# Optimization experiments

Measured on AMD Instinct MI355X. Metric: run time of the kernel, lower is better.

The kernel has to match this reference:

```python
import jax, jax.numpy as jnp
import numpy as np

D_MODEL = 2048
DOWN = 512
UP = 1024
NUM_HEADS = 16
ROPE_DIM = 64
BS = 16
SEQ = 512
BASE = 10000.0
HEAD_DIM = D_MODEL // NUM_HEADS          # 128 (used only in the softmax scale)
V_HEAD_DIM = UP // NUM_HEADS             # 64


def _linear(x, W, b):
    # torch nn.Linear: y = x @ W.T + b, W shape (out, in)
    return x @ W.T + b


def _rope(x, num_heads, rope_dim):
    # Faithful to source RotaryEmbedding, including the swapped sin/cos caches:
    #   cos_pos = sin(pos*theta), sin_pos = cos(pos*theta)
    bs, L, _ = x.shape
    q = x.reshape(bs, L, num_heads, rope_dim).transpose(0, 2, 1, 3)  # (bs,h,L,d)
    theta = 1.0 / (BASE ** (jnp.arange(0, rope_dim, 2, dtype=jnp.float32) / rope_dim))
    ang = jnp.arange(L, dtype=jnp.float32)[:, None] * theta[None, :]   # (L, d/2)
    cos_pos = jnp.repeat(jnp.sin(ang), 2, axis=-1)  # (L, d) -- source quirk
    sin_pos = jnp.repeat(jnp.cos(ang), 2, axis=-1)
    q2 = jnp.stack([-q[..., 1::2], q[..., ::2]], axis=-1).reshape(bs, num_heads, L, rope_dim)
    return q * cos_pos + q2 * sin_pos


def setup_inputs() -> dict:
    key = jax.random.key(0)
    ks = jax.random.split(key, 18)
    s = 0.02
    d = {
        "h": jax.random.normal(ks[0], (BS, SEQ, D_MODEL), jnp.float32),
        "W_down_kv": jax.random.normal(ks[1], (DOWN, D_MODEL), jnp.float32) * s,
        "b_down_kv": jnp.zeros((DOWN,), jnp.float32),
        "W_up_k": jax.random.normal(ks[2], (UP, DOWN), jnp.float32) * s,
        "b_up_k": jnp.zeros((UP,), jnp.float32),
        "W_up_v": jax.random.normal(ks[3], (UP, DOWN), jnp.float32) * s,
        "b_up_v": jnp.zeros((UP,), jnp.float32),
        "W_down_q": jax.random.normal(ks[4], (DOWN, D_MODEL), jnp.float32) * s,
        "b_down_q": jnp.zeros((DOWN,), jnp.float32),
        "W_up_q": jax.random.normal(ks[5], (UP, DOWN), jnp.float32) * s,
        "b_up_q": jnp.zeros((UP,), jnp.float32),
        "W_qr": jax.random.normal(ks[6], (ROPE_DIM * NUM_HEADS, DOWN), jnp.float32) * s,
        "b_qr": jnp.zeros((ROPE_DIM * NUM_HEADS,), jnp.float32),
        "W_kr": jax.random.normal(ks[7], (ROPE_DIM, D_MODEL), jnp.float32) * s,
        "b_kr": jnp.zeros((ROPE_DIM,), jnp.float32),
        "W_fc": jax.random.normal(ks[8], (D_MODEL, NUM_HEADS * V_HEAD_DIM), jnp.float32) * s,
        "b_fc": jnp.zeros((D_MODEL,), jnp.float32),
    }
    return d


def reference(h, W_down_kv, b_down_kv, W_up_k, b_up_k, W_up_v, b_up_v,
              W_down_q, b_down_q, W_up_q, b_up_q, W_qr, b_qr,
              W_kr, b_kr, W_fc, b_fc):
    bs, L, _ = h.shape
    # low-rank KV path
    c_kv = _linear(h, W_down_kv, b_down_kv)             # (bs,L,down)
    k_c = _linear(c_kv, W_up_k, b_up_k)                 # (bs,L,up)
    v_c = _linear(c_kv, W_up_v, b_up_v)                 # (bs,L,up)
    # low-rank Q path
    c_q = _linear(h, W_down_q, b_down_q)                # (bs,L,down)
    q_c = _linear(c_q, W_up_q, b_up_q)                  # (bs,L,up)
    # rope (decoupled) path
    q_r = _rope(_linear(c_q, W_qr, b_qr), NUM_HEADS, ROPE_DIM)  # (bs,H,L,rope)
    k_r = _rope(_linear(h, W_kr, b_kr), 1, ROPE_DIM)            # (bs,1,L,rope)

    q_c = q_c.reshape(bs, L, NUM_HEADS, -1).transpose(0, 2, 1, 3)  # (bs,H,L,64)
    q = jnp.concatenate([q_c, q_r], axis=-1)                        # (bs,H,L,128)
    k_c = k_c.reshape(bs, L, NUM_HEADS, -1).transpose(0, 2, 1, 3)
    k_r = jnp.broadcast_to(k_r, (bs, NUM_HEADS, L, ROPE_DIM))       # shared across heads
    k = jnp.concatenate([k_c, k_r], axis=-1)

    scale = 1.0 / jnp.sqrt(jnp.float32(HEAD_DIM + ROPE_DIM))  # sqrt(192), per source
    scores = jnp.einsum('bhqd,bhkd->bhqk', q, k) * scale
    attn = jax.nn.softmax(scores, axis=-1)  # dropout is identity in eval mode

    v = v_c.reshape(bs, L, NUM_HEADS, V_HEAD_DIM).transpose(0, 2, 1, 3)
    out = jnp.einsum('bhqk,bhkd->bhqd', attn, v)
    out = out.transpose(0, 2, 1, 3).reshape(bs, L, -1)   # (bs,L,H*v_head_dim)
    return _linear(out, W_fc, b_fc)                      # (bs,L,d_model)
```

## Files before the change

kernel.cpp:

```cpp
#include <hip/hip_runtime.h>
#include <hip/hip_bf16.h>

typedef __bf16 bf16x8 __attribute__((ext_vector_type(8)));
typedef float f32x4 __attribute__((ext_vector_type(4)));
using u16 = unsigned short;
using u32 = unsigned int;

__device__ __forceinline__ float bf2f(u16 v) {
    unsigned int u = (unsigned int)v << 16;
    float f; __builtin_memcpy(&f, &u, 4); return f;
}
__device__ __forceinline__ u16 f2bf(float f) {
    unsigned int u; __builtin_memcpy(&u, &f, 4);
    u += 0x7FFFu + ((u >> 16) & 1u);
    return (u16)(u >> 16);
}

struct Cvt9 {
    const float* src[9];
    u16* dst[9];
    int end[9];
};
__global__ __launch_bounds__(256) void cvt_all(Cvt9 d, int total)
{
    int c = blockIdx.x * 256 + threadIdx.x;
    if (c >= total) return;
    int seg = 0;
    while (c >= d.end[seg]) ++seg;
    int local = c - (seg ? d.end[seg - 1] : 0);
    const float* s = d.src[seg] + (size_t)local * 8;
    float4 f0 = *(const float4*)s;
    float4 f1 = *(const float4*)(s + 4);
    u16 tmp[8] = { f2bf(f0.x), f2bf(f0.y), f2bf(f0.z), f2bf(f0.w),
                   f2bf(f1.x), f2bf(f1.y), f2bf(f1.z), f2bf(f1.w) };
    *(uint4*)(d.dst[seg] + (size_t)local * 8) = *(const uint4*)tmp;
}

struct Cpy7 {
    const float* src[7];
    float* dst[7];
    int end[7];
};
__global__ __launch_bounds__(256) void copy_f32(Cpy7 d, int total)
{
    int c = blockIdx.x * 256 + threadIdx.x;
    if (c >= total) return;
    int seg = 0;
    while (c >= d.end[seg]) ++seg;
    int local = c - (seg ? d.end[seg - 1] : 0);
    d.dst[seg][local] = d.src[seg][local];
}

template<bool CF>
__global__ __launch_bounds__(256) void gemm_v6(
    const u16* __restrict__ A0, const u16* __restrict__ B0, void* __restrict__ C0, const float* __restrict__ e0,
    const u16* __restrict__ A1, const u16* __restrict__ B1, void* __restrict__ C1, const float* __restrict__ e1,
    int ysplit, int lda, int ldb, int ldc, int N, int K)
{
    __shared__ __align__(16) u16 As[3][128 * 32];
    __shared__ __align__(16) u16 Bs[3][128 * 32];

    const int t = threadIdx.x;
    const int lane = t & 63;
    const int w = t >> 6;
    const int wm = w >> 1, wn = w & 1;
    const int l16 = lane & 15, quad = lane >> 4;
    const int m0 = blockIdx.x * 128;

    const u16* A; const u16* B; void* Cv; const float* bias; int yl;
    if ((int)blockIdx.y < ysplit) { A = A0; B = B0; Cv = C0; bias = e0; yl = blockIdx.y; }
    else                          { A = A1; B = B1; Cv = C1; bias = e1; yl = blockIdx.y - ysplit; }
    const int n0 = yl * 128;

    const int sub  = lane >> 2;
    const int slot = lane & 3;
    const int agc  = slot ^ ((sub >> 1) & 3);
    const int sfr  = (l16 >> 1) & 3;

    f32x4 acc[4][4];
#pragma unroll
    for (int i = 0; i < 4; ++i)
#pragma unroll
        for (int j = 0; j < 4; ++j) acc[i][j] = (f32x4){0.f, 0.f, 0.f, 0.f};

    auto STAGE = [&](int buf, int k0) {
#pragma unroll
        for (int c = 0; c < 2; ++c) {
            const int rr = w * 32 + c * 16;
            const u16* ga = A + (size_t)(m0 + rr + sub) * lda + k0 + agc * 8;
            __builtin_amdgcn_global_load_lds(
                (const __attribute__((address_space(1))) u32*)ga,
                (__attribute__((address_space(3))) u32*)&As[buf][rr * 32], 16, 0, 0);
            const u16* gb = B + (size_t)(n0 + rr + sub) * ldb + k0 + agc * 8;
            __builtin_amdgcn_global_load_lds(
                (const __attribute__((address_space(1))) u32*)gb,
                (__attribute__((address_space(3))) u32*)&Bs[buf][rr * 32], 16, 0, 0);
        }
    };

    const int nt = K >> 5;
    STAGE(0, 0);
    STAGE(1, 32);
    int cur = 0;
    for (int tt = 0; tt < nt; ++tt) {
        int pre = cur + 2; if (pre >= 3) pre -= 3;
        if (tt + 2 < nt) {
            STAGE(pre, (tt + 2) << 5);
            asm volatile("s_waitcnt vmcnt(8)");
        } else if (tt + 1 < nt) {
            asm volatile("s_waitcnt vmcnt(4)");
        } else {
            asm volatile("s_waitcnt vmcnt(0)");
        }
        __builtin_amdgcn_s_barrier();

        const u16* Ab = As[cur];
        bf16x8 af[4], bfr[4];
#pragma unroll
        for (int i = 0; i < 4; ++i)
            af[i] = *(const bf16x8*)&Ab[(wm * 64 + i * 16 + l16) * 32 + (quad ^ sfr) * 8];
#pragma unroll
        for (int j = 0; j < 4; ++j)
            bfr[j] = *(const bf16x8*)&Bs[cur][(wn * 64 + j * 16 + l16) * 32 + (quad ^ sfr) * 8];
#pragma unroll
        for (int i = 0; i < 4; ++i)
#pragma unroll
            for (int j = 0; j < 4; ++j)
                acc[i][j] = __builtin_amdgcn_mfma_f32_16x16x32_bf16(bfr[j], af[i], acc[i][j], 0, 0, 0);

        __builtin_amdgcn_s_barrier();
        cur += 1; if (cur >= 3) cur -= 3;
    }

#pragma unroll
    for (int i = 0; i < 4; ++i) {
        const int row = m0 + wm * 64 + i * 16 + l16;
#pragma unroll
        for (int j = 0; j < 4; ++j) {
            const int colb = n0 + wn * 64 + j * 16 + quad * 4;
            if (colb >= N) continue;
            float4 bv = *(const float4*)&bias[colb];
            float v0 = acc[i][j][0] + bv.x;
            float v1 = acc[i][j][1] + bv.y;
            float v2 = acc[i][j][2] + bv.z;
            float v3 = acc[i][j][3] + bv.w;
            if (CF) {
                float4 out = { v0, v1, v2, v3 };
                *(float4*)((float*)Cv + (size_t)row * ldc + colb) = out;
            } else {
                u16 p[4] = { f2bf(v0), f2bf(v1), f2bf(v2), f2bf(v3) };
                *(uint2*)((u16*)Cv + (size_t)row * ldc + colb) = *(const uint2*)p;
            }
        }
    }
}

__global__ void rope_inplace(u16* __restrict__ buf, int ld, int col0, int ppr, int total)
{
    int idx = blockIdx.x * 256 + threadIdx.x;
    if (idx >= total) return;
    int row = idx / ppr;
    int pi  = idx - row * ppr;
    int grp = pi >> 5;
    int i   = pi & 31;
    int pos = row & 511;
    float theta = __expf(-(float)i * 0.2878231366242558f);
    float ang = (float)pos * theta;
    float s = sinf(ang), c = cosf(ang);
    size_t base = (size_t)row * ld + col0 + grp * 64 + 2 * i;
    float x0 = bf2f(buf[base]);
    float x1 = bf2f(buf[base + 1]);
    buf[base]     = f2bf(x0 * s - x1 * c);
    buf[base + 1] = f2bf(x1 * s + x0 * c);
}

__global__ __launch_bounds__(256) void attn_kernel(
    const u16* __restrict__ q_src,
    const u16* __restrict__ kv_src,
    const u16* __restrict__ kr_src,
    u16* __restrict__ o_dst, int ldo)
{
    __shared__ __align__(16) u16 Ks[64 * 136];
    __shared__ __align__(16) u16 Vt[64 * 72];
    __shared__ __align__(16) u16 Ps[64 * 72];

    const int t = threadIdx.x;
    const int lane = t & 63;
    const int w = t >> 6;
    const int l16 = lane & 15, quad = lane >> 4;
    const int a7 = l16 & 7;

    const int id   = blockIdx.x;
    const int xcd  = id & 7;
    const int qt   = (id >> 3) & 7;
    const int panel = xcd + ((id >> 6) << 3);
    const int h = panel & 15;
    const int b = panel >> 4;
    const int qrow0 = b * 512 + qt * 64;
    const int krow_base = b * 512;

    bf16x8 aq[4];
    {
        const u16* qrow = q_src + (size_t)(qrow0 + w * 16 + l16) * 2048;
#pragma unroll
        for (int ks = 0; ks < 4; ++ks) {
            int col = ks * 32 + quad * 8;
            const u16* src = (col < 64) ? qrow + h * 64 + col
                                        : qrow + 1024 + h * 64 + (col - 64);
            aq[ks] = *(const bf16x8*)src;
        }
    }

    const int colK = (t & 15) * 8;
    const int r0k  = t >> 4;
    const u16* kbase; int kstr;
    if (colK < 64) { kbase = kv_src + h * 64 + colK;        kstr = 2048; }
    else           { kbase = kr_src + 1024 + (colK - 64);   kstr = 1088; }
    u16* kw = &Ks[r0k * 136 + colK];

    const int v00 = (t & 7) * 8;
    const int r0v = t >> 3;
    const u16* vbase = kv_src + 1024 + h * 64 + v00;
    const int rotA = (r0v + v00) & 63;
    const int rotB = (r0v + 32 + v00) & 63;
    u16* vwA = &Vt[v00 * 72 + rotA];
    u16* vwB = &Vt[v00 * 72 + rotB];

    auto LOADT = [&](int krow0, uint4& K0, uint4& K1, uint4& K2, uint4& K3,
                     uint4& V0, uint4& V1) {
        K0 = *(const uint4*)(kbase + (size_t)(krow0 + r0k     ) * kstr);
        K1 = *(const uint4*)(kbase + (size_t)(krow0 + r0k + 16) * kstr);
        K2 = *(const uint4*)(kbase + (size_t)(krow0 + r0k + 32) * kstr);
        K3 = *(const uint4*)(kbase + (size_t)(krow0 + r0k + 48) * kstr);
        V0 = *(const uint4*)(vbase + (size_t)(krow0 + r0v     ) * 2048);
        V1 = *(const uint4*)(vbase + (size_t)(krow0 + r0v + 32) * 2048);
    };
    auto WRITET = [&](const uint4& K0, const uint4& K1, const uint4& K2, const uint4& K3,
                      const uint4& V0, const uint4& V1) {
        *(uint4*)(kw)            = K0;
        *(uint4*)(kw + 16 * 136) = K1;
        *(uint4*)(kw + 32 * 136) = K2;
        *(uint4*)(kw + 48 * 136) = K3;
        u16 ta[8], tb[8];
        __builtin_memcpy(ta, &V0, 16);
        __builtin_memcpy(tb, &V1, 16);
#pragma unroll
        for (int j2 = 0; j2 < 8; ++j2) { vwA[j2 * 72] = ta[j2]; vwB[j2 * 72] = tb[j2]; }
    };

    float m2 = -1e30f, l_run = 0.f;
    f32x4 o[4];
#pragma unroll
    for (int n = 0; n < 4; ++n) o[n] = (f32x4){0.f, 0.f, 0.f, 0.f};

    const float C = 0.10411756f;

    uint4 kA0, kA1, kA2, kA3, vA0, vA1;
    uint4 kB0, kB1, kB2, kB3, vB0, vB1;
    LOADT(krow_base, kA0, kA1, kA2, kA3, vA0, vA1);

    for (int kt = 0; kt < 8; ++kt) {
        __builtin_amdgcn_s_barrier();
        if ((kt & 1) == 0) {
            WRITET(kA0, kA1, kA2, kA3, vA0, vA1);
            if (kt < 7) LOADT(krow_base + (kt + 1) * 64, kB0, kB1, kB2, kB3, vB0, vB1);
        } else {
            WRITET(kB0, kB1, kB2, kB3, vB0, vB1);
            if (kt < 7) LOADT(krow_base + (kt + 1) * 64, kA0, kA1, kA2, kA3, vA0, vA1);
        }
        asm volatile("s_waitcnt lgkmcnt(0)");
        __builtin_amdgcn_sched_barrier(0);
        __builtin_amdgcn_s_barrier();

        f32x4 s[4];
#pragma unroll
        for (int n = 0; n < 4; ++n) s[n] = (f32x4){0.f, 0.f, 0.f, 0.f};
#pragma unroll
        for (int ks = 0; ks < 4; ++ks) {
#pragma unroll
            for (int n = 0; n < 4; ++n) {
                bf16x8 bk = *(const bf16x8*)&Ks[(n * 16 + l16) * 136 + ks * 32 + quad * 8];
                s[n] = __builtin_amdgcn_mfma_f32_16x16x32_bf16(bk, aq[ks], s[n], 0, 0, 0);
            }
        }

        float mx = fmaxf(fmaxf(s[0][0], s[0][1]), fmaxf(s[0][2], s[0][3]));
#pragma unroll
        for (int n = 1; n < 4; ++n)
            mx = fmaxf(mx, fmaxf(fmaxf(s[n][0], s[n][1]), fmaxf(s[n][2], s[n][3])));
        mx = fmaxf(mx, __shfl_xor(mx, 16));
        mx = fmaxf(mx, __shfl_xor(mx, 32));

        float mnew = fmaxf(m2, mx * C);
        float alpha = __builtin_amdgcn_exp2f(m2 - mnew);
        m2 = mnew;
        float rs = 0.f;
#pragma unroll
        for (int n = 0; n < 4; ++n)
#pragma unroll
            for (int r = 0; r < 4; ++r) {
                float pv = __builtin_amdgcn_exp2f(__builtin_fmaf(s[n][r], C, -mnew));
                s[n][r] = pv;
                rs += pv;
            }
        rs += __shfl_xor(rs, 16);
        rs += __shfl_xor(rs, 32);
        l_run = l_run * alpha + rs;

        float aO[4];
#pragma unroll
        for (int r = 0; r < 4; ++r) aO[r] = __shfl(alpha, quad * 4 + r);
#pragma unroll
        for (int n = 0; n < 4; ++n)
#pragma unroll
            for (int r = 0; r < 4; ++r) o[n][r] *= aO[r];

        {
            u16* prow = &Ps[(w * 16 + l16) * 72];
#pragma unroll
            for (int n = 0; n < 4; ++n) {
                int p = (2 * n + (quad >> 1) + a7) & 7;
                u32 p0 = (u32)f2bf(s[n][0]) | ((u32)f2bf(s[n][1]) << 16);
                u32 p1 = (u32)f2bf(s[n][2]) | ((u32)f2bf(s[n][3]) << 16);
                uint2 pp = { p0, p1 };
                *(uint2*)&prow[p * 8 + (quad & 1) * 4] = pp;
            }
        }

#pragma unroll
        for (int kk = 0; kk < 2; ++kk) {
            bf16x8 ap = *(const bf16x8*)&Ps[(w * 16 + l16) * 72
                          + (((4 * kk + quad + a7) & 7) << 3)];
#pragma unroll
            for (int n = 0; n < 4; ++n) {
                bf16x8 bv = *(const bf16x8*)&Vt[(n * 16 + l16) * 72
                              + ((kk * 32 + quad * 8 + n * 16 + (l16 & 8)) & 63)];
                o[n] = __builtin_amdgcn_mfma_f32_16x16x32_bf16(ap, bv, o[n], 0, 0, 0);
            }
        }
    }

    float inv = 1.0f / l_run;
#pragma unroll
    for (int r = 0; r < 4; ++r) {
        float invO = __shfl(inv, quad * 4 + r);
        int row = qrow0 + w * 16 + quad * 4 + r;
#pragma unroll
        for (int n = 0; n < 4; ++n) {
            int col = h * 64 + n * 16 + l16;
            o_dst[(size_t)row * ldo + col] = f2bf(o[n][r] * invO);
        }
    }
}

extern "C" void kernel_launch(void* const* d_in, const int* in_sizes, int n_in,
                              void* d_out, int out_size, void* d_ws, size_t ws_size,
                              hipStream_t stream)
{
    const float* h    = (const float*)d_in[0];
    const float* Wdkv = (const float*)d_in[1];
    const float* bdkv = (const float*)d_in[2];
    const float* Wuk  = (const float*)d_in[3];
    const float* buk  = (const float*)d_in[4];
    const float* Wuv  = (const float*)d_in[5];
    const float* buv  = (const float*)d_in[6];
    const float* Wdq  = (const float*)d_in[7];
    const float* bdq  = (const float*)d_in[8];
    const float* Wuq  = (const float*)d_in[9];
    const float* buq  = (const float*)d_in[10];
    const float* Wqr  = (const float*)d_in[11];
    const float* bqr  = (const float*)d_in[12];
    const float* Wkr  = (const float*)d_in[13];
    const float* bkr  = (const float*)d_in[14];
    const float* Wfc  = (const float*)d_in[15];
    const float* bfc  = (const float*)d_in[16];

    char* ws = (char*)d_ws;
    u16* out1   = (u16*)ws;
    u16* hbf    = (u16*)(ws + 17825792);
    u16* out2a  = hbf;
    u16* out2b  = (u16*)(ws + 51380224);
    u16* w1     = (u16*)(ws + 84934656);
    u16* w2a    = (u16*)(ws + 89653248);
    u16* w2b    = (u16*)(ws + 91750400);
    u16* wfc    = (u16*)(ws + 93847552);
    float* bias_s1 = (float*)(ws + 98041856);
    float* bias_2  = (float*)(ws + 98046208);

    Cvt9 cd;
    const float* srcs[9] = { h, Wdkv, Wdq, Wkr, Wuk, Wuv, Wuq, Wqr, Wfc };
    u16* dsts[9] = { hbf, w1, w1 + 512 * 2048, w1 + 1024 * 2048,
                     w2a, w2a + 1024 * 512, w2b, w2b + 1024 * 512, wfc };
    int cnts[9] = { 2097152, 131072, 131072, 16384, 65536, 65536, 65536, 65536, 262144 };
    int acc2 = 0;
    for (int i = 0; i < 9; ++i) { cd.src[i] = srcs[i]; cd.dst[i] = dsts[i]; acc2 += cnts[i]; cd.end[i] = acc2; }
    cvt_all<<<(acc2 + 255) / 256, 256, 0, stream>>>(cd, acc2);
    hipMemsetAsync(w1 + 1088 * 2048, 0, 64 * 2048 * sizeof(u16), stream);

    Cpy7 bc;
    const float* bs[7] = { bdkv, bdq, bkr, buk, buv, buq, bqr };
    float* bd[7] = { bias_s1, bias_s1 + 512, bias_s1 + 1024,
                     bias_2, bias_2 + 1024, bias_2 + 2048, bias_2 + 3072 };
    int bn[7] = { 512, 512, 64, 1024, 1024, 1024, 1024 };
    int bacc = 0;
    for (int i = 0; i < 7; ++i) { bc.src[i] = bs[i]; bc.dst[i] = bd[i]; bacc += bn[i]; bc.end[i] = bacc; }
    copy_f32<<<(bacc + 255) / 256, 256, 0, stream>>>(bc, bacc);

    gemm_v6<false><<<dim3(64, 9), 256, 0, stream>>>(
        hbf, w1, out1, bias_s1,
        hbf, w1, out1, bias_s1, 9, 2048, 2048, 1088, 1088, 2048);
    rope_inplace<<<1024, 256, 0, stream>>>(out1, 1088, 1024, 32, 8192 * 32);

    gemm_v6<false><<<dim3(64, 32), 256, 0, stream>>>(
        out1,       w2a, out2a, bias_2,
        out1 + 512, w2b, out2b, bias_2 + 2048, 16, 1088, 512, 2048, 2048, 512);
    rope_inplace<<<16384, 256, 0, stream>>>(out2b, 2048, 1024, 512, 8192 * 512);

    attn_kernel<<<2048, 256, 0, stream>>>(out2b, out2a, out1, out1, 1088);

    gemm_v6<true><<<dim3(64, 16), 256, 0, stream>>>(
        out1, wfc, d_out, bfc,
        out1, wfc, d_out, bfc, 16, 1088, 1024, 2048, 2048, 1024);
}
```

Measured before the change: 414.3 us.

## Fuse RoPE into GEMM epilogues, widen attention blocks, skip rescale when max stable

The two standalone rope_inplace passes are removed, and RoPE is applied in the GEMM epilogue to columns at or above 1024, computed in fp32 before the bf16 rounding. The attention kernel now runs 512 threads over 128 query rows, so each K/V tile is shared by twice as many queries and each thread issues fewer loads. The online softmax skips the max update and output rescale when the new tile max stays within a threshold of the running max, trading exactness of the running max for fewer exp and multiply operations. These changes remove extra memory passes and kernel launches, but the lazy-rescale threshold risks overflow or precision loss if scores jump sharply.

```diff
diff --git a/kernel.cpp b/kernel.cpp
--- a/kernel.cpp
+++ b/kernel.cpp
@@ -52,10 +52,10 @@
 }
 
 template<bool CF>
-__global__ __launch_bounds__(256) void gemm_v6(
+__global__ __launch_bounds__(256) void gemm_v7(
     const u16* __restrict__ A0, const u16* __restrict__ B0, void* __restrict__ C0, const float* __restrict__ e0,
     const u16* __restrict__ A1, const u16* __restrict__ B1, void* __restrict__ C1, const float* __restrict__ e1,
-    int ysplit, int lda, int ldb, int ldc, int N, int K)
+    int ysplit, int lda, int ldb, int ldc, int N, int K, int rp0, int rp1)
 {
     __shared__ __align__(16) u16 As[3][128 * 32];
     __shared__ __align__(16) u16 Bs[3][128 * 32];
@@ -67,9 +67,9 @@
     const int l16 = lane & 15, quad = lane >> 4;
     const int m0 = blockIdx.x * 128;
 
-    const u16* A; const u16* B; void* Cv; const float* bias; int yl;
-    if ((int)blockIdx.y < ysplit) { A = A0; B = B0; Cv = C0; bias = e0; yl = blockIdx.y; }
-    else                          { A = A1; B = B1; Cv = C1; bias = e1; yl = blockIdx.y - ysplit; }
+    const u16* A; const u16* B; void* Cv; const float* bias; int yl; int rp;
+    if ((int)blockIdx.y < ysplit) { A = A0; B = B0; Cv = C0; bias = e0; yl = blockIdx.y; rp = rp0; }
+    else                          { A = A1; B = B1; Cv = C1; bias = e1; yl = blockIdx.y - ysplit; rp = rp1; }
     const int n0 = yl * 128;
 
     const int sub  = lane >> 2;
@@ -144,6 +144,21 @@
             float v1 = acc[i][j][1] + bv.y;
             float v2 = acc[i][j][2] + bv.z;
             float v3 = acc[i][j][3] + bv.w;
+            if (rp && colb >= 1024) {
+                const float LN = 0.2878231366242558f;
+                int i0 = ((colb - 1024) & 63) >> 1;
+                float th0 = __expf(-(float)i0 * LN);
+                float th1 = __expf(-(float)(i0 + 1) * LN);
+                float ps = (float)(row & 511);
+                float a0 = ps * th0, a1 = ps * th1;
+                float s0 = sinf(a0), c0 = cosf(a0);
+                float s1 = sinf(a1), c1 = cosf(a1);
+                float t0 = v0 * s0 - v1 * c0;
+                float t1 = v1 * s0 + v0 * c0;
+                float t2 = v2 * s1 - v3 * c1;
+                float t3 = v3 * s1 + v2 * c1;
+                v0 = t0; v1 = t1; v2 = t2; v3 = t3;
+            }
             if (CF) {
                 float4 out = { v0, v1, v2, v3 };
                 *(float4*)((float*)Cv + (size_t)row * ldc + colb) = out;
@@ -155,26 +170,7 @@
     }
 }
 
-__global__ void rope_inplace(u16* __restrict__ buf, int ld, int col0, int ppr, int total)
-{
-    int idx = blockIdx.x * 256 + threadIdx.x;
-    if (idx >= total) return;
-    int row = idx / ppr;
-    int pi  = idx - row * ppr;
-    int grp = pi >> 5;
-    int i   = pi & 31;
-    int pos = row & 511;
-    float theta = __expf(-(float)i * 0.2878231366242558f);
-    float ang = (float)pos * theta;
-    float s = sinf(ang), c = cosf(ang);
-    size_t base = (size_t)row * ld + col0 + grp * 64 + 2 * i;
-    float x0 = bf2f(buf[base]);
-    float x1 = bf2f(buf[base + 1]);
-    buf[base]     = f2bf(x0 * s - x1 * c);
-    buf[base + 1] = f2bf(x1 * s + x0 * c);
-}
-
-__global__ __launch_bounds__(256) void attn_kernel(
+__global__ __launch_bounds__(512) void attn_kernel(
     const u16* __restrict__ q_src,
     const u16* __restrict__ kv_src,
     const u16* __restrict__ kr_src,
@@ -182,7 +178,7 @@
 {
     __shared__ __align__(16) u16 Ks[64 * 136];
     __shared__ __align__(16) u16 Vt[64 * 72];
-    __shared__ __align__(16) u16 Ps[64 * 72];
+    __shared__ __align__(16) u16 Ps[128 * 72];
 
     const int t = threadIdx.x;
     const int lane = t & 63;
@@ -192,11 +188,11 @@
 
     const int id   = blockIdx.x;
     const int xcd  = id & 7;
-    const int qt   = (id >> 3) & 7;
-    const int panel = xcd + ((id >> 6) << 3);
+    const int qt   = (id >> 3) & 3;
+    const int panel = xcd + ((id >> 5) << 3);
     const int h = panel & 15;
     const int b = panel >> 4;
-    const int qrow0 = b * 512 + qt * 64;
+    const int qrow0 = b * 512 + qt * 128;
     const int krow_base = b * 512;
 
     bf16x8 aq[4];
@@ -222,30 +218,20 @@
     const int r0v = t >> 3;
     const u16* vbase = kv_src + 1024 + h * 64 + v00;
     const int rotA = (r0v + v00) & 63;
-    const int rotB = (r0v + 32 + v00) & 63;
     u16* vwA = &Vt[v00 * 72 + rotA];
-    u16* vwB = &Vt[v00 * 72 + rotB];
-
-    auto LOADT = [&](int krow0, uint4& K0, uint4& K1, uint4& K2, uint4& K3,
-                     uint4& V0, uint4& V1) {
+
+    auto LOADT = [&](int krow0, uint4& K0, uint4& K1, uint4& V0) {
         K0 = *(const uint4*)(kbase + (size_t)(krow0 + r0k     ) * kstr);
-        K1 = *(const uint4*)(kbase + (size_t)(krow0 + r0k + 16) * kstr);
-        K2 = *(const uint4*)(kbase + (size_t)(krow0 + r0k + 32) * kstr);
-        K3 = *(const uint4*)(kbase + (size_t)(krow0 + r0k + 48) * kstr);
+        K1 = *(const uint4*)(kbase + (size_t)(krow0 + r0k + 32) * kstr);
         V0 = *(const uint4*)(vbase + (size_t)(krow0 + r0v     ) * 2048);
-        V1 = *(const uint4*)(vbase + (size_t)(krow0 + r0v + 32) * 2048);
     };
-    auto WRITET = [&](const uint4& K0, const uint4& K1, const uint4& K2, const uint4& K3,
-                      const uint4& V0, const uint4& V1) {
+    auto WRITET = [&](const uint4& K0, const uint4& K1, const uint4& V0) {
         *(uint4*)(kw)            = K0;
-        *(uint4*)(kw + 16 * 136) = K1;
-        *(uint4*)(kw + 32 * 136) = K2;
-        *(uint4*)(kw + 48 * 136) = K3;
-        u16 ta[8], tb[8];
+        *(uint4*)(kw + 32 * 136) = K1;
+        u16 ta[8];
         __builtin_memcpy(ta, &V0, 16);
-        __builtin_memcpy(tb, &V1, 16);
-#pragma unroll
-        for (int j2 = 0; j2 < 8; ++j2) { vwA[j2 * 72] = ta[j2]; vwB[j2 * 72] = tb[j2]; }
+#pragma unroll
+        for (int j2 = 0; j2 < 8; ++j2) vwA[j2 * 72] = ta[j2];
     };
 
     float m2 = -1e30f, l_run = 0.f;
@@ -254,19 +240,20 @@
     for (int n = 0; n < 4; ++n) o[n] = (f32x4){0.f, 0.f, 0.f, 0.f};
 
     const float C = 0.10411756f;
-
-    uint4 kA0, kA1, kA2, kA3, vA0, vA1;
-    uint4 kB0, kB1, kB2, kB3, vB0, vB1;
-    LOADT(krow_base, kA0, kA1, kA2, kA3, vA0, vA1);
+    const float THR2 = 11.5419f;
+
+    uint4 kA0, kA1, vA0;
+    uint4 kB0, kB1, vB0;
+    LOADT(krow_base, kA0, kA1, vA0);
 
     for (int kt = 0; kt < 8; ++kt) {
         __builtin_amdgcn_s_barrier();
         if ((kt & 1) == 0) {
-            WRITET(kA0, kA1, kA2, kA3, vA0, vA1);
-            if (kt < 7) LOADT(krow_base + (kt + 1) * 64, kB0, kB1, kB2, kB3, vB0, vB1);
+            WRITET(kA0, kA1, vA0);
+            if (kt < 7) LOADT(krow_base + (kt + 1) * 64, kB0, kB1, vB0);
         } else {
-            WRITET(kB0, kB1, kB2, kB3, vB0, vB1);
-            if (kt < 7) LOADT(krow_base + (kt + 1) * 64, kA0, kA1, kA2, kA3, vA0, vA1);
+            WRITET(kB0, kB1, vB0);
+            if (kt < 7) LOADT(krow_base + (kt + 1) * 64, kA0, kA1, vA0);
         }
         asm volatile("s_waitcnt lgkmcnt(0)");
         __builtin_amdgcn_sched_barrier(0);
@@ -290,30 +277,46 @@
             mx = fmaxf(mx, fmaxf(fmaxf(s[n][0], s[n][1]), fmaxf(s[n][2], s[n][3])));
         mx = fmaxf(mx, __shfl_xor(mx, 16));
         mx = fmaxf(mx, __shfl_xor(mx, 32));
-
-        float mnew = fmaxf(m2, mx * C);
-        float alpha = __builtin_amdgcn_exp2f(m2 - mnew);
-        m2 = mnew;
-        float rs = 0.f;
-#pragma unroll
-        for (int n = 0; n < 4; ++n)
-#pragma unroll
-            for (int r = 0; r < 4; ++r) {
-                float pv = __builtin_amdgcn_exp2f(__builtin_fmaf(s[n][r], C, -mnew));
-                s[n][r] = pv;
-                rs += pv;
-            }
-        rs += __shfl_xor(rs, 16);
-        rs += __shfl_xor(rs, 32);
-        l_run = l_run * alpha + rs;
-
-        float aO[4];
-#pragma unroll
-        for (int r = 0; r < 4; ++r) aO[r] = __shfl(alpha, quad * 4 + r);
-#pragma unroll
-        for (int n = 0; n < 4; ++n)
-#pragma unroll
-            for (int r = 0; r < 4; ++r) o[n][r] *= aO[r];
+        float mxC = mx * C;
+
+        if (__all(mxC <= m2 + THR2)) {
+            float rs = 0.f;
+#pragma unroll
+            for (int n = 0; n < 4; ++n)
+#pragma unroll
+                for (int r = 0; r < 4; ++r) {
+                    float pv = __builtin_amdgcn_exp2f(__builtin_fmaf(s[n][r], C, -m2));
+                    s[n][r] = pv;
+                    rs += pv;
+                }
+            rs += __shfl_xor(rs, 16);
+            rs += __shfl_xor(rs, 32);
+            l_run += rs;
+        } else {
+            float mnew = fmaxf(m2, mxC);
+            float alpha = __builtin_amdgcn_exp2f(m2 - mnew);
+            m2 = mnew;
+            float rs = 0.f;
+#pragma unroll
+            for (int n = 0; n < 4; ++n)
+#pragma unroll
+                for (int r = 0; r < 4; ++r) {
+                    float pv = __builtin_amdgcn_exp2f(__builtin_fmaf(s[n][r], C, -mnew));
+                    s[n][r] = pv;
+                    rs += pv;
+                }
+            rs += __shfl_xor(rs, 16);
+            rs += __shfl_xor(rs, 32);
+            l_run = l_run * alpha + rs;
+
+            float aO[4];
+#pragma unroll
+            for (int r = 0; r < 4; ++r) aO[r] = __shfl(alpha, quad * 4 + r);
+#pragma unroll
+            for (int n = 0; n < 4; ++n)
+#pragma unroll
+                for (int r = 0; r < 4; ++r) o[n][r] *= aO[r];
+        }
 
         {
             u16* prow = &Ps[(w * 16 + l16) * 72];
@@ -406,19 +409,17 @@
     for (int i = 0; i < 7; ++i) { bc.src[i] = bs[i]; bc.dst[i] = bd[i]; bacc += bn[i]; bc.end[i] = bacc; }
     copy_f32<<<(bacc + 255) / 256, 256, 0, stream>>>(bc, bacc);
 
-    gemm_v6<false><<<dim3(64, 9), 256, 0, stream>>>(
+    gemm_v7<false><<<dim3(64, 9), 256, 0, stream>>>(
         hbf, w1, out1, bias_s1,
-        hbf, w1, out1, bias_s1, 9, 2048, 2048, 1088, 1088, 2048);
-    rope_inplace<<<1024, 256, 0, stream>>>(out1, 1088, 1024, 32, 8192 * 32);
-
-    gemm_v6<false><<<dim3(64, 32), 256, 0, stream>>>(
+        hbf, w1, out1, bias_s1, 9, 2048, 2048, 1088, 1088, 2048, 1, 1);
+
+    gemm_v7<false><<<dim3(64, 32), 256, 0, stream>>>(
         out1,       w2a, out2a, bias_2,
-        out1 + 512, w2b, out2b, bias_2 + 2048, 16, 1088, 512, 2048, 2048, 512);
-    rope_inplace<<<16384, 256, 0, stream>>>(out2b, 2048, 1024, 512, 8192 * 512);
-
-    attn_kernel<<<2048, 256, 0, stream>>>(out2b, out2a, out1, out1, 1088);
-
-    gemm_v6<true><<<dim3(64, 16), 256, 0, stream>>>(
+        out1 + 512, w2b, out2b, bias_2 + 2048, 16, 1088, 512, 2048, 2048, 512, 0, 1);
+
+    attn_kernel<<<1024, 512, 0, stream>>>(out2b, out2a, out1, out1, 1088);
+
+    gemm_v7<true><<<dim3(64, 16), 256, 0, stream>>>(
         out1, wfc, d_out, bfc,
-        out1, wfc, d_out, bfc, 16, 1088, 1024, 2048, 2048, 1024);
-}
+        out1, wfc, d_out, bfc, 16, 1088, 1024, 2048, 2048, 1024, 0, 0);
+}
```

New measurement: 432.0 us. +4.3%, slower.
